# Optimization experiments

Hardware: AMD Instinct MI355X
Metric: run time of the kernel (lower is better)

## Reference

```python
import jax, jax.numpy as jnp
import numpy as np

# ---- polar grid config (matches init_kwargs) ----
N_RADIAL = 48
N_ANGULAR = 72
RADIAL_EDGES = jnp.arange(2.0, 51.0, dtype=jnp.float32)            # 49 edges, [2, 50] m
ANGLE_EDGES = jnp.linspace(-np.pi, np.pi, N_ANGULAR + 1).astype(jnp.float32)
Z_MIN, Z_MAX = -3.0, 5.0
MAX_PTS = 64      # max_points_per_voxel
MAX_VOX = 3000    # max_voxels (< H = 3456, truncation path active)
H = N_RADIAL * N_ANGULAR


def setup_inputs() -> dict:
    key = jax.random.key(0)
    pts = jax.random.normal(key, (4_000_000, 5), dtype=jnp.float32)
    # scale xy to ~[-45,45] m and z to ~[-6,6] m so masks keep a realistic fraction
    scale = jnp.array([15.0, 15.0, 2.0, 1.0, 1.0], dtype=jnp.float32)
    return {"points": pts * scale}


def reference(points):
    N, C = points.shape
    x, y, z = points[:, 0], points[:, 1], points[:, 2]
    r = jnp.sqrt(x * x + y * y)
    theta = jnp.arctan2(y, x)

    valid = ((z >= Z_MIN) & (z < Z_MAX)
             & (r >= RADIAL_EDGES[0]) & (r < RADIAL_EDGES[-1])
             & (theta >= ANGLE_EDGES[0]) & (theta < ANGLE_EDGES[-1]))

    # torch.searchsorted(right=False) == jnp side='left'
    r_idx = jnp.clip(jnp.searchsorted(RADIAL_EDGES, r, side='left') - 1, 0, N_RADIAL - 1)
    t_idx = jnp.clip(jnp.searchsorted(ANGLE_EDGES, theta, side='left') - 1, 0, N_ANGULAR - 1)

    # invalid points get sentinel hash H (out of range -> dropped by scatter)
    vhash = jnp.where(valid, r_idx * N_ANGULAR + t_idx, H).astype(jnp.int32)

    # sort points by voxel hash (stable, matching torch.argsort semantics here)
    order = jnp.argsort(vhash)
    sh = vhash[order]                       # [N] sorted hashes
    sp = points[order]                      # [N, C] points in hash order

    # rank of each point within its voxel = position - first occurrence of its hash
    first = jnp.searchsorted(sh, sh, side='left')
    rank = jnp.arange(N, dtype=jnp.int32) - first.astype(jnp.int32)

    # dense hard-voxelization scatter: keep first MAX_PTS points per voxel.
    # out-of-range (sh==H or rank>=MAX_PTS) indices are dropped.
    vox_dense = jnp.zeros((H, MAX_PTS, C), dtype=points.dtype).at[sh, rank].set(sp, mode='drop')

    counts = jax.ops.segment_sum(jnp.ones_like(vhash), vhash, num_segments=H + 1)[:H]
    npts_dense = jnp.minimum(counts, MAX_PTS).astype(jnp.int32)

    # unique occupied hashes in ascending order -> output slots (first MAX_VOX kept)
    occupied = counts > 0
    slot = jnp.cumsum(occupied.astype(jnp.int32)) - 1
    slot = jnp.where(occupied & (slot < MAX_VOX), slot, MAX_VOX)  # MAX_VOX => dropped
    slot2hash = jnp.zeros((MAX_VOX,), jnp.int32).at[slot].set(jnp.arange(H, dtype=jnp.int32), mode='drop')
    slot_valid = jnp.zeros((MAX_VOX,), bool).at[slot].set(True, mode='drop')

    voxels = jnp.where(slot_valid[:, None, None], vox_dense[slot2hash], 0.0)  # [MAX_VOX, MAX_PTS, C]
    num_points = jnp.where(slot_valid, npts_dense[slot2hash], 0)

    ri = slot2hash // N_ANGULAR
    ti = slot2hash % N_ANGULAR
    coords = jnp.where(slot_valid[:, None],
                       jnp.stack([ri, ti, jnp.zeros_like(ri)], axis=1), 0).astype(jnp.int32)

    r_c = 0.5 * (RADIAL_EDGES[ri] + RADIAL_EDGES[ri + 1])
    t_c = 0.5 * (ANGLE_EDGES[ti] + ANGLE_EDGES[ti + 1])
    centers = jnp.where(slot_valid[:, None],
                        jnp.stack([r_c * jnp.cos(t_c), r_c * jnp.sin(t_c)], axis=1), 0.0)

    return voxels, coords, num_points, centers
```

## Files before the change

### kernel.cpp

```cpp
#include <hip/hip_runtime.h>
#include <math.h>

#define NRAD 48
#define NANG 72
#define HV   3456
#define HVW  864
#define MAXP 64
#define MAXV 3000
#define BLK  256
#define CHT  64
#define TILE 4096
#define SUBT 1024
#define NCH  16

#define OFF_C   (MAXV*MAXP*5)
#define OFF_N   (OFF_C + MAXV*3)
#define OFF_X   (OFF_N + MAXV)

#define PI_F 3.14159265358979323846f

__device__ __forceinline__ float angle_edge(int j) {
  const double PI = 3.14159265358979311599796346854;
  const double step = (PI - (-PI)) / 72.0;
  if (j == 72) return (float)PI;
  return (float)(-PI + (double)j * step);
}

__device__ __forceinline__ int point_bin(float x, float y, float z,
                                         const float* __restrict__ eang) {
  float r = __fsqrt_rn(__fadd_rn(__fmul_rn(x, x), __fmul_rn(y, y)));
  if (!(z >= -3.0f && z < 5.0f && r >= 2.0f && r < 50.0f)) return HV;
  int ri = (int)ceilf(r) - 3;
  ri = max(0, min(NRAD - 1, ri));
  float ax = fabsf(x), ay = fabsf(y);
  float u = fminf(ax, ay), U = fmaxf(ax, ay);
  bool big = u > 0.41421356f * U;
  float num = big ? (U - u) : u;
  float den = big ? (U + u) : U;
  float v = num / den;
  float s = v * v;
  float a = 0.05882353f;
  a = a * s - 0.06666667f;
  a = a * s + 0.07692308f;
  a = a * s - 0.09090909f;
  a = a * s + 0.11111111f;
  a = a * s - 0.14285714f;
  a = a * s + 0.2f;
  a = a * s - 0.33333333f;
  a = a * s + 1.0f;
  float pp = v * a;
  float th1 = big ? (0.78539816f - pp) : pp;
  if (ay > ax) th1 = 1.57079633f - th1;
  if (x < 0.0f) th1 = PI_F - th1;
  float that = copysignf(th1, y);
  int g = (int)floorf((that + PI_F) * 11.459155902616465f);
  g = max(0, min(NANG - 1, g));
  while (g > 0 && !(eang[g] < that)) g--;
  while (g < NANG - 1 && eang[g + 1] < that) g++;
  float d0 = that - eang[g];
  float d1 = eang[g + 1] - that;
  const float GUARD = 2e-5f;
  if (d0 > GUARD && d1 > GUARD) return ri * NANG + g;
  float th = (float)atan2((double)y, (double)x);
  if (!(th >= eang[0] && th < eang[72])) return HV;
  int gg = g;
  while (gg > 0 && !(eang[gg] < th)) gg--;
  while (gg < NANG - 1 && eang[gg + 1] < th) gg++;
  return ri * NANG + max(0, min(NANG - 1, gg));
}

__global__ __launch_bounds__(BLK) void k_hist(
    const float* __restrict__ pts, int N, int tile, int n4, int tailN,
    unsigned char* __restrict__ hist, unsigned short* __restrict__ bins,
    float4* __restrict__ out4) {
  __shared__ int lh[HV];
  __shared__ float eang[73];
  int t = blockIdx.x, tid = threadIdx.x;
  for (int j = t * BLK + tid; j < n4; j += gridDim.x * BLK)
    out4[j] = make_float4(0.f, 0.f, 0.f, 0.f);
  if (t == 0 && tid < tailN) ((float*)out4)[(size_t)n4 * 4 + tid] = 0.f;
  for (int i = tid; i < HV; i += BLK) lh[i] = 0;
  if (tid < 73) eang[tid] = angle_edge(tid);
  __syncthreads();
  int base = t * tile;
  int end  = min(base + tile, N);
  int endq = base + (((end - base) >> 2) << 2);
  const float4* p4 = (const float4*)pts;
  for (int i0 = base + (tid << 2); i0 < endq; i0 += (BLK << 2)) {
    size_t q = (size_t)(i0 >> 2) * 5;
    float4 v0 = p4[q], v1 = p4[q + 1], v2 = p4[q + 2], v3 = p4[q + 3], v4 = p4[q + 4];
    int b0 = point_bin(v0.x, v0.y, v0.z, eang);
    int b1 = point_bin(v1.y, v1.z, v1.w, eang);
    int b2 = point_bin(v2.z, v2.w, v3.x, eang);
    int b3 = point_bin(v3.w, v4.x, v4.y, eang);
    *(ushort4*)(bins + i0) = make_ushort4((unsigned short)b0, (unsigned short)b1,
                                          (unsigned short)b2, (unsigned short)b3);
    if (b0 < HV) atomicAdd(&lh[b0], 1);
    if (b1 < HV) atomicAdd(&lh[b1], 1);
    if (b2 < HV) atomicAdd(&lh[b2], 1);
    if (b3 < HV) atomicAdd(&lh[b3], 1);
  }
  for (int i = endq + tid; i < end; i += BLK) {
    size_t p = (size_t)i * 5;
    int b = point_bin(pts[p], pts[p + 1], pts[p + 2], eang);
    bins[i] = (unsigned short)b;
    if (b < HV) atomicAdd(&lh[b], 1);
  }
  __syncthreads();
  unsigned char* ht = hist + (size_t)t * HV;
  for (int i = tid; i < HV; i += BLK) ht[i] = (unsigned char)min(lh[i], 64);
}

__global__ void k_scan_a(const unsigned int* __restrict__ hist32, int NT,
                         unsigned int* __restrict__ part32) {
  int w = blockIdx.x * BLK + threadIdx.x;
  int c = blockIdx.y;
  if (w >= HVW) return;
  int t0 = c * CHT, t1 = min(t0 + CHT, NT);
  int s0 = 0, s1 = 0, s2 = 0, s3 = 0;
  for (int t = t0; t < t1; ++t) {
    unsigned int v = hist32[(size_t)t * HVW + w];
    s0 = min(s0 + (int)(v & 255u), 64);
    s1 = min(s1 + (int)((v >> 8) & 255u), 64);
    s2 = min(s2 + (int)((v >> 16) & 255u), 64);
    s3 = min(s3 + (int)(v >> 24), 64);
  }
  part32[(size_t)c * HVW + w] = (unsigned)s0 | ((unsigned)s1 << 8) |
                                ((unsigned)s2 << 16) | ((unsigned)s3 << 24);
}

__global__ __launch_bounds__(1024) void k_bsc(unsigned int* __restrict__ part32, int NC,
                                              int* __restrict__ soh,
                                              float* __restrict__ out) {
  __shared__ float eang[73];
  __shared__ int ssum[1024];
  int tid = threadIdx.x;
  if (tid < 73) eang[tid] = angle_edge(tid);
  int r0 = 0, r1 = 0, r2 = 0, r3 = 0;
  for (int cb = 0; cb < NC; cb += 16) {
    unsigned int vv[16];
#pragma unroll
    for (int k = 0; k < 16; ++k) {
      int c = cb + k;
      vv[k] = (tid < HVW && c < NC) ? part32[(size_t)c * HVW + tid] : 0u;
    }
#pragma unroll
    for (int k = 0; k < 16; ++k) {
      int c = cb + k;
      if (tid < HVW && c < NC)
        part32[(size_t)c * HVW + tid] = (unsigned)r0 | ((unsigned)r1 << 8) |
                                        ((unsigned)r2 << 16) | ((unsigned)r3 << 24);
      r0 = min(r0 + (int)(vv[k] & 255u), 64);
      r1 = min(r1 + (int)((vv[k] >> 8) & 255u), 64);
      r2 = min(r2 + (int)((vv[k] >> 16) & 255u), 64);
      r3 = min(r3 + (int)(vv[k] >> 24), 64);
    }
  }
  int c0 = r0, c1 = r1, c2 = r2, c3 = r3;
  int occ = (c0 > 0) + (c1 > 0) + (c2 > 0) + (c3 > 0);
  if (tid >= HVW) occ = 0;
  ssum[tid] = occ;
  __syncthreads();
  for (int off = 1; off < 1024; off <<= 1) {
    int v = (tid >= off) ? ssum[tid - off] : 0;
    __syncthreads();
    ssum[tid] += v;
    __syncthreads();
  }
  int base = ssum[tid] - occ;
  if (tid < HVW) {
    int cs[4] = {c0, c1, c2, c3};
#pragma unroll
    for (int k = 0; k < 4; ++k) {
      int h = tid * 4 + k;
      int cnt = cs[k];
      int s = -1;
      if (cnt > 0) {
        if (base < MAXV) s = base;
        base++;
      }
      soh[h] = s;
      if (s >= 0) {
        int ri = h / NANG, ti = h % NANG;
        out[OFF_C + s * 3 + 0] = (float)ri;
        out[OFF_C + s * 3 + 1] = (float)ti;
        out[OFF_C + s * 3 + 2] = 0.0f;
        out[OFF_N + s] = (float)cnt;
        float rc = 2.5f + (float)ri;
        float tc = 0.5f * (eang[ti] + eang[ti + 1]);
        out[OFF_X + s * 2 + 0] = rc * cosf(tc);
        out[OFF_X + s * 2 + 1] = rc * sinf(tc);
      }
    }
  }
}

__global__ void k_scan_c(unsigned int* __restrict__ hist32, int NT,
                         const unsigned int* __restrict__ part32) {
  int w = blockIdx.x * BLK + threadIdx.x;
  int c = blockIdx.y;
  if (w >= HVW) return;
  int t0 = c * CHT, t1 = min(t0 + CHT, NT);
  unsigned int pv = part32[(size_t)c * HVW + w];
  int r0 = pv & 255u, r1 = (pv >> 8) & 255u, r2 = (pv >> 16) & 255u, r3 = pv >> 24;
  for (int t = t0; t < t1; ++t) {
    size_t o = (size_t)t * HVW + w;
    unsigned int v = hist32[o];
    hist32[o] = (unsigned)r0 | ((unsigned)r1 << 8) |
                ((unsigned)r2 << 16) | ((unsigned)r3 << 24);
    r0 = min(r0 + (int)(v & 255u), 64);
    r1 = min(r1 + (int)((v >> 8) & 255u), 64);
    r2 = min(r2 + (int)((v >> 16) & 255u), 64);
    r3 = min(r3 + (int)(v >> 24), 64);
  }
}

__global__ __launch_bounds__(BLK) void k_scatter_fast(
    const float* __restrict__ pts, int N,
    const unsigned char* __restrict__ hist, const unsigned short* __restrict__ bins,
    const int* __restrict__ soh, float* __restrict__ out) {
  __shared__ unsigned int whd[4 * HV / 2];
  unsigned short (*wh)[HV] = (unsigned short (*)[HV])whd;
  int t = blockIdx.x;
  int tid = threadIdx.x;
  int lane = tid & 63, wv = tid >> 6;
  for (int i = tid; i < 4 * HV / 2; i += BLK) whd[i] = 0u;
  __syncthreads();
  int base = t * TILE;
  int end  = min(base + TILE, N);
  int sb = base + wv * SUBT;
  int se = min(sb + SUBT, end);
  const unsigned char* ht = hist + (size_t)t * HV;
  unsigned short lb[NCH], lr[NCH];
  const unsigned long long lmask = (1ULL << lane) - 1ULL;
#pragma unroll
  for (int c = 0; c < NCH; ++c) {
    int i = sb + c * 64 + lane;
    int b = 4095;
    if (i < se) {
      int bi = bins[i];
      if (bi < HV && ht[bi] < 64) b = bi;
    }
    lb[c] = (unsigned short)b;
    lr[c] = 0;
    if (__ballot(b != 4095) == 0ULL) continue;
    unsigned long long m = ~0ULL;
#pragma unroll
    for (int k = 0; k < 12; ++k) {
      unsigned long long bal = __ballot((b >> k) & 1);
      m &= ((b >> k) & 1) ? bal : ~bal;
    }
    int rho = __popcll(m & lmask);
    int kap = __popcll(m);
    int cv = 0;
    if (b != 4095) {
      cv = wh[wv][b];
      if (rho == 0) wh[wv][b] = (unsigned short)(cv + kap);
    }
    lr[c] = (unsigned short)(cv + rho);
  }
  __syncthreads();
  for (int j = tid; j < HV; j += BLK) {
    int a0 = wh[0][j], a1 = wh[1][j], a2 = wh[2][j];
    wh[0][j] = 0;
    wh[1][j] = (unsigned short)a0;
    wh[2][j] = (unsigned short)(a0 + a1);
    wh[3][j] = (unsigned short)(a0 + a1 + a2);
  }
  __syncthreads();
#pragma unroll
  for (int c = 0; c < NCH; ++c) {
    int b = lb[c];
    if (b == 4095) continue;
    int rank = (int)ht[b] + (int)wh[wv][b] + (int)lr[c];
    if (rank < MAXP) {
      int s = soh[b];
      if (s >= 0) {
        int i = sb + c * 64 + lane;
        size_t dst = (size_t)(s * MAXP + rank) * 5;
        size_t src = (size_t)i * 5;
        out[dst + 0] = pts[src + 0];
        out[dst + 1] = pts[src + 1];
        out[dst + 2] = pts[src + 2];
        out[dst + 3] = pts[src + 3];
        out[dst + 4] = pts[src + 4];
      }
    }
  }
}

__global__ void k_scatter_gen(const float* __restrict__ pts, int N, int tile,
                              const unsigned char* __restrict__ hist,
                              const unsigned short* __restrict__ bins,
                              const int* __restrict__ soh,
                              float* __restrict__ out) {
  __shared__ int cur[HV + 1];
  int t = blockIdx.x;
  int tid = threadIdx.x;
  const unsigned char* ht = hist + (size_t)t * HV;
  for (int i = tid; i < HV + 1; i += BLK) cur[i] = (i < HV) ? (int)ht[i] : 0;
  __syncthreads();
  int base = t * tile;
  int end  = min(base + tile, N);
  int lane = tid & 63, wv = tid >> 6;
  for (int g = base; g < base + tile; g += BLK) {
    int i = g + tid;
    bool act = (i < end);
    int b = act ? (int)bins[i] : 0x10000;
    int rho = 0, kap = 0;
    for (int j = 0; j < 64; ++j) {
      int bj = __shfl(b, j, 64);
      if (bj == b) { kap++; if (j < lane) rho++; }
    }
    int rank = 0x7FFFFFFF;
    for (int w = 0; w < 4; ++w) {
      if (wv == w && act) {
        int bs = cur[b];
        rank = bs + rho;
        if (rho == 0) cur[b] = bs + kap;
      }
      __syncthreads();
    }
    if (act && rank < MAXP && b < HV) {
      int s = soh[b];
      if (s >= 0) {
        size_t dst = (size_t)(s * MAXP + rank) * 5;
        size_t src = (size_t)i * 5;
        out[dst + 0] = pts[src + 0];
        out[dst + 1] = pts[src + 1];
        out[dst + 2] = pts[src + 2];
        out[dst + 3] = pts[src + 3];
        out[dst + 4] = pts[src + 4];
      }
    }
  }
}

extern "C" void kernel_launch(void* const* d_in, const int* in_sizes, int n_in,
                              void* d_out, int out_size, void* d_ws, size_t ws_size,
                              hipStream_t stream) {
  const float* pts = (const float*)d_in[0];
  int N = in_sizes[0] / 5;
  float* out = (float*)d_out;

  auto align = [](size_t x) { return (x + 255) & ~(size_t)255; };
  int tile = TILE, NT = 1, NC = 1;
  size_t o_hist = 0, o_part = 0, o_soh = 0, o_bins = 0;
  for (;;) {
    NT = (N + tile - 1) / tile;
    NC = (NT + CHT - 1) / CHT;
    o_hist = 0;
    o_part = align(o_hist + (size_t)NT * HV);
    o_soh  = align(o_part + (size_t)NC * HV);
    o_bins = align(o_soh + (size_t)HV * 4);
    size_t need = o_bins + (size_t)N * 2;
    if (need <= ws_size || tile >= (1 << 22)) break;
    tile <<= 1;
  }

  char* w = (char*)d_ws;
  unsigned char* hist = (unsigned char*)(w + o_hist);
  unsigned int*  hist32 = (unsigned int*)hist;
  unsigned int*  part32 = (unsigned int*)(w + o_part);
  int* soh = (int*)(w + o_soh);
  unsigned short* bins = (unsigned short*)(w + o_bins);

  int n4 = out_size / 4;
  int tailN = out_size - n4 * 4;

  k_hist<<<NT, BLK, 0, stream>>>(pts, N, tile, n4, tailN, hist, bins, (float4*)out);
  dim3 ga((HVW + BLK - 1) / BLK, NC);
  k_scan_a<<<ga, BLK, 0, stream>>>(hist32, NT, part32);
  k_bsc<<<1, 1024, 0, stream>>>(part32, NC, soh, out);
  k_scan_c<<<ga, BLK, 0, stream>>>(hist32, NT, part32);
  if (tile == TILE) {
    k_scatter_fast<<<NT, BLK, 0, stream>>>(pts, N, hist, bins, soh, out);
  } else {
    k_scatter_gen<<<NT, BLK, 0, stream>>>(pts, N, tile, hist, bins, soh, out);
  }
}
```

Measured before the change: 92.00 us.

## Fuse three scan kernels into one kernel with inter-block flag synchronization

```diff
diff --git a/kernel.cpp b/kernel.cpp
--- a/kernel.cpp
+++ b/kernel.cpp
@@ -72,13 +72,14 @@
 __global__ __launch_bounds__(BLK) void k_hist(
     const float* __restrict__ pts, int N, int tile, int n4, int tailN,
     unsigned char* __restrict__ hist, unsigned short* __restrict__ bins,
-    float4* __restrict__ out4) {
+    float4* __restrict__ out4, int* __restrict__ flags) {
   __shared__ int lh[HV];
   __shared__ float eang[73];
   int t = blockIdx.x, tid = threadIdx.x;
   for (int j = t * BLK + tid; j < n4; j += gridDim.x * BLK)
     out4[j] = make_float4(0.f, 0.f, 0.f, 0.f);
   if (t == 0 && tid < tailN) ((float*)out4)[(size_t)n4 * 4 + tid] = 0.f;
+  if (t == 0 && tid >= 64 && tid < 96) flags[tid - 64] = 0;
   for (int i = tid; i < HV; i += BLK) lh[i] = 0;
   if (tid < 73) eang[tid] = angle_edge(tid);
   __syncthreads();
@@ -111,107 +112,103 @@
   for (int i = tid; i < HV; i += BLK) ht[i] = (unsigned char)min(lh[i], 64);
 }
 
-__global__ void k_scan_a(const unsigned int* __restrict__ hist32, int NT,
-                         unsigned int* __restrict__ part32) {
-  int w = blockIdx.x * BLK + threadIdx.x;
-  int c = blockIdx.y;
-  if (w >= HVW) return;
-  int t0 = c * CHT, t1 = min(t0 + CHT, NT);
-  int s0 = 0, s1 = 0, s2 = 0, s3 = 0;
-  for (int t = t0; t < t1; ++t) {
-    unsigned int v = hist32[(size_t)t * HVW + w];
-    s0 = min(s0 + (int)(v & 255u), 64);
-    s1 = min(s1 + (int)((v >> 8) & 255u), 64);
-    s2 = min(s2 + (int)((v >> 16) & 255u), 64);
-    s3 = min(s3 + (int)(v >> 24), 64);
-  }
-  part32[(size_t)c * HVW + w] = (unsigned)s0 | ((unsigned)s1 << 8) |
-                                ((unsigned)s2 << 16) | ((unsigned)s3 << 24);
-}
-
-__global__ __launch_bounds__(1024) void k_bsc(unsigned int* __restrict__ part32, int NC,
-                                              int* __restrict__ soh,
-                                              float* __restrict__ out) {
-  __shared__ float eang[73];
-  __shared__ int ssum[1024];
+__global__ __launch_bounds__(1024) void k_scan2(
+    unsigned int* __restrict__ hist32, int NT, int NC,
+    unsigned int* __restrict__ part32, int* flags,
+    int* __restrict__ soh, float* __restrict__ out) {
+  int c = blockIdx.x;
   int tid = threadIdx.x;
-  if (tid < 73) eang[tid] = angle_edge(tid);
-  int r0 = 0, r1 = 0, r2 = 0, r3 = 0;
-  for (int cb = 0; cb < NC; cb += 16) {
-    unsigned int vv[16];
+  if (c < NC) {
+    int t0 = c * CHT, t1 = min(t0 + CHT, NT);
+    if (tid < HVW) {
+      int s0 = 0, s1 = 0, s2 = 0, s3 = 0;
+      for (int t = t0; t < t1; ++t) {
+        unsigned int v = hist32[(size_t)t * HVW + tid];
+        s0 = min(s0 + (int)(v & 255u), 64);
+        s1 = min(s1 + (int)((v >> 8) & 255u), 64);
+        s2 = min(s2 + (int)((v >> 16) & 255u), 64);
+        s3 = min(s3 + (int)(v >> 24), 64);
+      }
+      part32[(size_t)c * HVW + tid] = (unsigned)s0 | ((unsigned)s1 << 8) |
+                                      ((unsigned)s2 << 16) | ((unsigned)s3 << 24);
+    }
+    __threadfence();
+    __syncthreads();
+    if (tid == 0) atomicExch(&flags[c], 1);
+    if (tid < NC) { while (atomicAdd(&flags[tid], 0) == 0) {} }
+    __threadfence();
+    __syncthreads();
+    if (tid < HVW) {
+      int r0 = 0, r1 = 0, r2 = 0, r3 = 0;
+      for (int cc = 0; cc < c; ++cc) {
+        unsigned int v = part32[(size_t)cc * HVW + tid];
+        r0 = min(r0 + (int)(v & 255u), 64);
+        r1 = min(r1 + (int)((v >> 8) & 255u), 64);
+        r2 = min(r2 + (int)((v >> 16) & 255u), 64);
+        r3 = min(r3 + (int)(v >> 24), 64);
+      }
+      for (int t = t0; t < t1; ++t) {
+        size_t o = (size_t)t * HVW + tid;
+        unsigned int v = hist32[o];
+        hist32[o] = (unsigned)r0 | ((unsigned)r1 << 8) |
+                    ((unsigned)r2 << 16) | ((unsigned)r3 << 24);
+        r0 = min(r0 + (int)(v & 255u), 64);
+        r1 = min(r1 + (int)((v >> 8) & 255u), 64);
+        r2 = min(r2 + (int)((v >> 16) & 255u), 64);
+        r3 = min(r3 + (int)(v >> 24), 64);
+      }
+    }
+  } else {
+    __shared__ int ssum[1024];
+    if (tid < NC) { while (atomicAdd(&flags[tid], 0) == 0) {} }
+    __threadfence();
+    __syncthreads();
+    int c0 = 0, c1 = 0, c2 = 0, c3 = 0;
+    if (tid < HVW) {
+      for (int cc = 0; cc < NC; ++cc) {
+        unsigned int v = part32[(size_t)cc * HVW + tid];
+        c0 = min(c0 + (int)(v & 255u), 64);
+        c1 = min(c1 + (int)((v >> 8) & 255u), 64);
+        c2 = min(c2 + (int)((v >> 16) & 255u), 64);
+        c3 = min(c3 + (int)(v >> 24), 64);
+      }
+    }
+    int occ = (c0 > 0) + (c1 > 0) + (c2 > 0) + (c3 > 0);
+    ssum[tid] = occ;
+    __syncthreads();
+    for (int off = 1; off < 1024; off <<= 1) {
+      int v = (tid >= off) ? ssum[tid - off] : 0;
+      __syncthreads();
+      ssum[tid] += v;
+      __syncthreads();
+    }
+    int base = ssum[tid] - occ;
+    if (tid < HVW) {
+      int cs[4] = {c0, c1, c2, c3};
 #pragma unroll
-    for (int k = 0; k < 16; ++k) {
-      int c = cb + k;
-      vv[k] = (tid < HVW && c < NC) ? part32[(size_t)c * HVW + tid] : 0u;
-    }
-#pragma unroll
-    for (int k = 0; k < 16; ++k) {
-      int c = cb + k;
-      if (tid < HVW && c < NC)
-        part32[(size_t)c * HVW + tid] = (unsigned)r0 | ((unsigned)r1 << 8) |
-                                        ((unsigned)r2 << 16) | ((unsigned)r3 << 24);
-      r0 = min(r0 + (int)(vv[k] & 255u), 64);
-      r1 = min(r1 + (int)((vv[k] >> 8) & 255u), 64);
-      r2 = min(r2 + (int)((vv[k] >> 16) & 255u), 64);
-      r3 = min(r3 + (int)(vv[k] >> 24), 64);
-    }
-  }
-  int c0 = r0, c1 = r1, c2 = r2, c3 = r3;
-  int occ = (c0 > 0) + (c1 > 0) + (c2 > 0) + (c3 > 0);
-  if (tid >= HVW) occ = 0;
-  ssum[tid] = occ;
-  __syncthreads();
-  for (int off = 1; off < 1024; off <<= 1) {
-    int v = (tid >= off) ? ssum[tid - off] : 0;
-    __syncthreads();
-    ssum[tid] += v;
-    __syncthreads();
-  }
-  int base = ssum[tid] - occ;
-  if (tid < HVW) {
-    int cs[4] = {c0, c1, c2, c3};
-#pragma unroll
-    for (int k = 0; k < 4; ++k) {
-      int h = tid * 4 + k;
-      int cnt = cs[k];
-      int s = -1;
-      if (cnt > 0) {
-        if (base < MAXV) s = base;
-        base++;
-      }
-      soh[h] = s;
-      if (s >= 0) {
-        int ri = h / NANG, ti = h % NANG;
-        out[OFF_C + s * 3 + 0] = (float)ri;
-        out[OFF_C + s * 3 + 1] = (float)ti;
-        out[OFF_C + s * 3 + 2] = 0.0f;
-        out[OFF_N + s] = (float)cnt;
-        float rc = 2.5f + (float)ri;
-        float tc = 0.5f * (eang[ti] + eang[ti + 1]);
-        out[OFF_X + s * 2 + 0] = rc * cosf(tc);
-        out[OFF_X + s * 2 + 1] = rc * sinf(tc);
-      }
-    }
-  }
-}
-
-__global__ void k_scan_c(unsigned int* __restrict__ hist32, int NT,
-                         const unsigned int* __restrict__ part32) {
-  int w = blockIdx.x * BLK + threadIdx.x;
-  int c = blockIdx.y;
-  if (w >= HVW) return;
-  int t0 = c * CHT, t1 = min(t0 + CHT, NT);
-  unsigned int pv = part32[(size_t)c * HVW + w];
-  int r0 = pv & 255u, r1 = (pv >> 8) & 255u, r2 = (pv >> 16) & 255u, r3 = pv >> 24;
-  for (int t = t0; t < t1; ++t) {
-    size_t o = (size_t)t * HVW + w;
-    unsigned int v = hist32[o];
-    hist32[o] = (unsigned)r0 | ((unsigned)r1 << 8) |
-                ((unsigned)r2 << 16) | ((unsigned)r3 << 24);
-    r0 = min(r0 + (int)(v & 255u), 64);
-    r1 = min(r1 + (int)((v >> 8) & 255u), 64);
-    r2 = min(r2 + (int)((v >> 16) & 255u), 64);
-    r3 = min(r3 + (int)(v >> 24), 64);
+      for (int k = 0; k < 4; ++k) {
+        int h = tid * 4 + k;
+        int cnt = cs[k];
+        int s = -1;
+        if (cnt > 0) {
+          if (base < MAXV) s = base;
+          base++;
+        }
+        soh[h] = s;
+        if (s >= 0) {
+          int ri = h / NANG, ti = h % NANG;
+          out[OFF_C + s * 3 + 0] = (float)ri;
+          out[OFF_C + s * 3 + 1] = (float)ti;
+          out[OFF_C + s * 3 + 2] = 0.0f;
+          out[OFF_N + s] = (float)cnt;
+          float rc = 2.5f + (float)ri;
+          float e0 = angle_edge(ti), e1 = angle_edge(ti + 1);
+          float tc = 0.5f * (e0 + e1);
+          out[OFF_X + s * 2 + 0] = rc * cosf(tc);
+          out[OFF_X + s * 2 + 1] = rc * sinf(tc);
+        }
+      }
+    }
   }
 }
 
@@ -345,14 +342,15 @@
 
   auto align = [](size_t x) { return (x + 255) & ~(size_t)255; };
   int tile = TILE, NT = 1, NC = 1;
-  size_t o_hist = 0, o_part = 0, o_soh = 0, o_bins = 0;
+  size_t o_hist = 0, o_part = 0, o_soh = 0, o_flag = 0, o_bins = 0;
   for (;;) {
     NT = (N + tile - 1) / tile;
     NC = (NT + CHT - 1) / CHT;
     o_hist = 0;
     o_part = align(o_hist + (size_t)NT * HV);
     o_soh  = align(o_part + (size_t)NC * HV);
-    o_bins = align(o_soh + (size_t)HV * 4);
+    o_flag = align(o_soh + (size_t)HV * 4);
+    o_bins = align(o_flag + 256);
     size_t need = o_bins + (size_t)N * 2;
     if (need <= ws_size || tile >= (1 << 22)) break;
     tile <<= 1;
@@ -362,17 +360,16 @@
   unsigned char* hist = (unsigned char*)(w + o_hist);
   unsigned int*  hist32 = (unsigned int*)hist;
   unsigned int*  part32 = (unsigned int*)(w + o_part);
-  int* soh = (int*)(w + o_soh);
+  int* soh   = (int*)(w + o_soh);
+  int* flags = (int*)(w + o_flag);
   unsigned short* bins = (unsigned short*)(w + o_bins);
 
   int n4 = out_size / 4;
   int tailN = out_size - n4 * 4;
 
-  k_hist<<<NT, BLK, 0, stream>>>(pts, N, tile, n4, tailN, hist, bins, (float4*)out);
-  dim3 ga((HVW + BLK - 1) / BLK, NC);
-  k_scan_a<<<ga, BLK, 0, stream>>>(hist32, NT, part32);
-  k_bsc<<<1, 1024, 0, stream>>>(part32, NC, soh, out);
-  k_scan_c<<<ga, BLK, 0, stream>>>(hist32, NT, part32);
+  k_hist<<<NT, BLK, 0, stream>>>(pts, N, tile, n4, tailN, hist, bins,
+                                 (float4*)out, flags);
+  k_scan2<<<NC + 1, 1024, 0, stream>>>(hist32, NT, NC, part32, flags, soh, out);
   if (tile == TILE) {
     k_scatter_fast<<<NT, BLK, 0, stream>>>(pts, N, hist, bins, soh, out);
   } else {
```

Measured after the change: 97.49 us. 6.0% more time.
